# Kernel optimization log

Measured on AMD Instinct MI355X. Metric: run time of the kernel, lower is better.

The kernel has to match this reference:

```python
import jax, jax.numpy as jnp
import numpy as np
import math

DIM = 768
HEADS = 12
HEAD_DIM = DIM // HEADS
LENS_T = 64
LENS_S = 256
NTOK = LENS_T + LENS_S
BATCH = 32
MLP_HIDDEN = 4 * DIM
KEEP_RATIO = 0.7
LENS_KEEP = math.ceil(KEEP_RATIO * LENS_S)  # 180, static
NEG_INF = -1e9  # finite stand-in for masked_fill(-inf); mask is all-False here
LN_EPS = 1e-5


def layer_norm(x, g, b):
    m = jnp.mean(x, axis=-1, keepdims=True)
    v = jnp.var(x, axis=-1, keepdims=True)
    return (x - m) * jax.lax.rsqrt(v + LN_EPS) * g + b


def attention(x_normed, w_qkv, w_proj, b_proj, mask):
    # x_normed: [B,N,C]; torch: qkv Linear (no bias), split heads, softmax(qk*scale), proj
    B, N, C = x_normed.shape
    qkv = (x_normed @ w_qkv.T).reshape(B, N, 3, HEADS, HEAD_DIM)
    qkv = jnp.transpose(qkv, (2, 0, 3, 1, 4))  # [3,B,H,N,Dh]
    q, k, v = qkv[0], qkv[1], qkv[2]
    scores = jnp.einsum('bhqd,bhkd->bhqk', q, k) * (HEAD_DIM ** -0.5)
    scores = jnp.where(mask[:, None, None, :], NEG_INF, scores)
    attn = jax.nn.softmax(scores, axis=-1)  # [B,H,N,N]
    out = jnp.einsum('bhqk,bhkd->bhqd', attn, v)
    out = jnp.transpose(out, (0, 2, 1, 3)).reshape(B, N, C)
    return out @ w_proj.T + b_proj, attn


def mlp(x, w_fc1, b_fc1, w_fc2, b_fc2):
    h = jax.nn.gelu(x @ w_fc1.T + b_fc1, approximate=False)
    return h @ w_fc2.T + b_fc2


def candidate_topk(attn_all, tmpl_mask_f):
    # attn_all: [B,H,N,N]; template->search block, masked mean over template rows,
    # mean over heads, sort descending, split into keep/removed.
    attn_ts = attn_all[:, :, :LENS_T, LENS_T:]  # [B,H,T,S]
    w = tmpl_mask_f[:, None, :, None]  # [B,1,T,1]
    denom = jnp.sum(tmpl_mask_f, axis=1)[:, None, None]  # [B,1,1]
    scores = jnp.sum(attn_ts * w, axis=2) / denom  # [B,H,S] mean over kept template rows
    scores = jnp.mean(scores, axis=1)  # [B,S] mean over heads
    order = jnp.argsort(-scores, axis=1)  # descending
    return order[:, :LENS_KEEP], order[:, LENS_KEEP:]


def gather_tokens(tokens, topk_idx):
    tokens_t = tokens[:, :LENS_T]
    tokens_s = tokens[:, LENS_T:]
    kept = jnp.take_along_axis(tokens_s, topk_idx[:, :, None], axis=1)
    return jnp.concatenate([tokens_t, kept], axis=1)


def setup_inputs() -> dict:
    key = jax.random.key(0)
    ks = jax.random.split(key, 12)
    s = 0.02
    return {
        'x_rgb': jax.random.normal(ks[0], (BATCH, NTOK, DIM), jnp.float32),
        'x_tir': jax.random.normal(ks[1], (BATCH, NTOK, DIM), jnp.float32),
        'global_index_t': jax.random.randint(ks[2], (BATCH, LENS_T), 0, 64).astype(jnp.int64),
        'global_index_s': jax.random.randint(ks[3], (BATCH, LENS_S), 0, 256).astype(jnp.int64),
        'mask': jnp.zeros((BATCH, NTOK), dtype=bool),
        'cte_template_mask': jnp.ones((BATCH, LENS_T), dtype=bool),
        'keep_ratio_search': 0,
        'js_loss': jax.random.normal(ks[4], (1,), jnp.float32),
        'g1': jnp.ones((DIM,), jnp.float32),
        'b1': jnp.zeros((DIM,), jnp.float32),
        'w_qkv': jax.random.normal(ks[5], (3 * DIM, DIM), jnp.float32) * s,
        'w_proj': jax.random.normal(ks[6], (DIM, DIM), jnp.float32) * s,
        'b_proj': jnp.zeros((DIM,), jnp.float32),
        'g2': jnp.ones((DIM,), jnp.float32),
        'b2': jnp.zeros((DIM,), jnp.float32),
        'w_fc1': jax.random.normal(ks[7], (MLP_HIDDEN, DIM), jnp.float32) * s,
        'b_fc1': jnp.zeros((MLP_HIDDEN,), jnp.float32),
        'w_fc2': jax.random.normal(ks[8], (DIM, MLP_HIDDEN), jnp.float32) * s,
        'b_fc2': jnp.zeros((DIM,), jnp.float32),
    }


def reference(x_rgb, x_tir, global_index_t, global_index_s, mask, cte_template_mask,
              keep_ratio_search, js_loss, g1, b1, w_qkv, w_proj, b_proj, g2, b2,
              w_fc1, b_fc1, w_fc2, b_fc2):
    # dual-stream shared-weight attention
    rgb_attn_out, corrmap_rgb = attention(layer_norm(x_rgb, g1, b1), w_qkv, w_proj, b_proj, mask)
    tir_attn_out, corrmap_tir = attention(layer_norm(x_tir, g1, b1), w_qkv, w_proj, b_proj, mask)
    x_rgb = x_rgb + rgb_attn_out  # drop_path = Identity
    x_tir = x_tir + tir_attn_out

    # candidate elimination: both streams use the SAME fused attention map,
    # so the topk is identical for rgb and tir (torch calls it twice, same result)
    attn_all = corrmap_rgb + corrmap_tir
    tmpl_mask_f = cte_template_mask.astype(attn_all.dtype)
    topk_idx, non_topk_idx = candidate_topk(attn_all, tmpl_mask_f)
    x_rgb = gather_tokens(x_rgb, topk_idx)
    x_tir = gather_tokens(x_tir, topk_idx)
    global_index_s_new = jnp.take_along_axis(global_index_s, topk_idx, axis=1)
    removed_index_s = jnp.take_along_axis(global_index_s, non_topk_idx, axis=1)

    x_rgb = x_rgb + mlp(layer_norm(x_rgb, g2, b2), w_fc1, b_fc1, w_fc2, b_fc2)
    x_tir = x_tir + mlp(layer_norm(x_tir, g2, b2), w_fc1, b_fc1, w_fc2, b_fc2)
    return (x_rgb, x_tir, global_index_t, global_index_s_new, removed_index_s,
            corrmap_rgb, corrmap_tir, js_loss)
```

## Files before the change

kernel.cpp:

```cpp
#include <hip/hip_runtime.h>

typedef long long LL;
typedef unsigned short ushort_t;
typedef __attribute__((ext_vector_type(8))) short bfrag;
typedef __attribute__((ext_vector_type(8))) _Float16 hfrag;
typedef __attribute__((ext_vector_type(4))) float facc;
typedef __attribute__((ext_vector_type(4))) unsigned short us4;

constexpr int CDIM  = 768;
constexpr int HEADS = 12;
constexpr int LT    = 64;
constexpr int NTOK  = 320;
constexpr int BATCH = 32;
constexpr int LKEEP = 180;
constexpr int LREM  = 76;
constexpr int NK    = 244;

constexpr LL O_XRGB = 0;
constexpr LL O_XTIR = 5996544;
constexpr LL O_GIT  = 11993088;
constexpr LL O_GSN  = 11995136;
constexpr LL O_REM  = 12000896;
constexpr LL O_CR   = 12003328;
constexpr LL O_CT   = 51324928;
constexpr LL O_JS   = 90646528;

constexpr LL W_X1   = 0;
constexpr LL W_X1G  = 15728640;
constexpr LL W_SC   = 27721728;
constexpr LL W_ORD  = 27738112;
constexpr LL W_XN   = 27746304;
constexpr LL W_QKV  = 35610624;
constexpr LL W_ATT  = 59596800;

constexpr LL SZH = 7864320;

__device__ inline ushort_t cvt_bf16(float f) {
    union { float f; unsigned u; } x; x.f = f;
    unsigned u = x.u + 0x7fffu + ((x.u >> 16) & 1u);
    return (ushort_t)(u >> 16);
}
union h16u { _Float16 h; ushort_t u; };

#define GLL(gp, lp) __builtin_amdgcn_global_load_lds( \
    (const __attribute__((address_space(1))) unsigned int*)(gp), \
    (__attribute__((address_space(3))) unsigned int*)(lp), 16, 0, 0)

template<bool B16OUT>
__global__ __launch_bounds__(256)
void ln_kernel(const float* __restrict__ x, const float* __restrict__ g,
               const float* __restrict__ bta, void* __restrict__ y)
{
    LL row = blockIdx.x;
    const float* xr = x + row * 768;
    int t = threadIdx.x;
    float v0 = xr[t], v1 = xr[t + 256], v2 = xr[t + 512];
    __shared__ float red[256];
    red[t] = v0 + v1 + v2;
    __syncthreads();
    for (int s = 128; s; s >>= 1) { if (t < s) red[t] += red[t + s]; __syncthreads(); }
    float mean = red[0] / 768.0f;
    __syncthreads();
    float d0 = v0 - mean, d1 = v1 - mean, d2 = v2 - mean;
    red[t] = d0 * d0 + d1 * d1 + d2 * d2;
    __syncthreads();
    for (int s = 128; s; s >>= 1) { if (t < s) red[t] += red[t + s]; __syncthreads(); }
    float var = red[0] / 768.0f;
    float rs = 1.0f / sqrtf(var + 1e-5f);
    float o0 = d0 * rs * g[t]       + bta[t];
    float o1 = d1 * rs * g[t + 256] + bta[t + 256];
    float o2 = d2 * rs * g[t + 512] + bta[t + 512];
    if (B16OUT) {
        ushort_t* yr = (ushort_t*)y + row * 768;
        yr[t] = cvt_bf16(o0); yr[t + 256] = cvt_bf16(o1); yr[t + 512] = cvt_bf16(o2);
    } else {
        float* yr = (float*)y + row * 768;
        yr[t] = o0; yr[t + 256] = o1; yr[t + 512] = o2;
    }
}

__global__ __launch_bounds__(256)
void ln_gather(const float* __restrict__ X1, const int* __restrict__ srcmap,
               const float* __restrict__ g, const float* __restrict__ bta,
               ushort_t* __restrict__ y)
{
    int row = blockIdx.x;
    const float* xr = X1 + (LL)srcmap[row] * 768;
    int t = threadIdx.x;
    float v0 = xr[t], v1 = xr[t + 256], v2 = xr[t + 512];
    __shared__ float red[256];
    red[t] = v0 + v1 + v2;
    __syncthreads();
    for (int s = 128; s; s >>= 1) { if (t < s) red[t] += red[t + s]; __syncthreads(); }
    float mean = red[0] / 768.0f;
    __syncthreads();
    float d0 = v0 - mean, d1 = v1 - mean, d2 = v2 - mean;
    red[t] = d0 * d0 + d1 * d1 + d2 * d2;
    __syncthreads();
    for (int s = 128; s; s >>= 1) { if (t < s) red[t] += red[t + s]; __syncthreads(); }
    float var = red[0] / 768.0f;
    float rs = 1.0f / sqrtf(var + 1e-5f);
    ushort_t* yr = y + (LL)row * 768;
    yr[t]       = cvt_bf16(d0 * rs * g[t]       + bta[t]);
    yr[t + 256] = cvt_bf16(d1 * rs * g[t + 256] + bta[t + 256]);
    yr[t + 512] = cvt_bf16(d2 * rs * g[t + 512] + bta[t + 512]);
}

__global__ __launch_bounds__(256)
void ln_f16x2(const float* __restrict__ x, const float* __restrict__ g,
              const float* __restrict__ bta,
              ushort_t* __restrict__ yh, ushort_t* __restrict__ yl)
{
    LL row = blockIdx.x;
    const float* xr = x + row * 768;
    int t = threadIdx.x;
    float v0 = xr[t], v1 = xr[t + 256], v2 = xr[t + 512];
    __shared__ float red[256];
    red[t] = v0 + v1 + v2;
    __syncthreads();
    for (int s = 128; s; s >>= 1) { if (t < s) red[t] += red[t + s]; __syncthreads(); }
    float mean = red[0] / 768.0f;
    __syncthreads();
    float d0 = v0 - mean, d1 = v1 - mean, d2 = v2 - mean;
    red[t] = d0 * d0 + d1 * d1 + d2 * d2;
    __syncthreads();
    for (int s = 128; s; s >>= 1) { if (t < s) red[t] += red[t + s]; __syncthreads(); }
    float var = red[0] / 768.0f;
    float rs = 1.0f / sqrtf(var + 1e-5f);
    #pragma unroll
    for (int c = 0; c < 3; ++c) {
        float d = (c == 0 ? d0 : c == 1 ? d1 : d2);
        int idx = t + c * 256;
        float o = d * rs * g[idx] + bta[idx];
        h16u hi, lo;
        hi.h = (_Float16)o;
        lo.h = (_Float16)(o - (float)hi.h);
        yh[row * 768 + idx] = hi.u;
        yl[row * 768 + idx] = lo.u;
    }
}

__global__ __launch_bounds__(256)
void cvt_f16x2(const float* __restrict__ in, ushort_t* __restrict__ oh,
               ushort_t* __restrict__ ol, int n)
{
    int i = (blockIdx.x * 256 + threadIdx.x) * 4;
    if (i >= n) return;
    float4 v = *(const float4*)(in + i);
    us4 h, l;
    #pragma unroll
    for (int j = 0; j < 4; ++j) {
        float f = (j == 0 ? v.x : j == 1 ? v.y : j == 2 ? v.z : v.w);
        h16u hh, ll;
        hh.h = (_Float16)f;
        ll.h = (_Float16)(f - (float)hh.h);
        h[j] = hh.u; l[j] = ll.u;
    }
    *(us4*)(oh + i) = h;
    *(us4*)(ol + i) = l;
}

__global__ __launch_bounds__(256)
void gemm_qkv(const ushort_t* __restrict__ Ah, const ushort_t* __restrict__ Al,
              const ushort_t* __restrict__ Bh, const ushort_t* __restrict__ Bl,
              ushort_t* __restrict__ Q1, ushort_t* __restrict__ Q2,
              ushort_t* __restrict__ K1, ushort_t* __restrict__ K2,
              ushort_t* __restrict__ Vt)
{
    __shared__ ushort_t Ahs[8192], Als[8192], Bhs[8192], Bls[8192];
    const int t = threadIdx.x;
    const int wave = t >> 6, lane = t & 63;
    const int wr = wave >> 1, wc = wave & 1;
    const int lr = lane & 15, lh = lane >> 4;
    const LL bm = (LL)blockIdx.y * 128, bn = (LL)blockIdx.x * 128;
    const bool vt = (blockIdx.x >= 12);

    facc acc[4][4];
    #pragma unroll
    for (int i = 0; i < 4; ++i)
        #pragma unroll
        for (int j = 0; j < 4; ++j) acc[i][j] = (facc)(0.0f);

    const LL soff = (bm + wave * 16 + (lane >> 2)) * (LL)768 + (lane & 3) * 8;
    const LL boff = (bn + wave * 16 + (lane >> 2)) * (LL)768 + (lane & 3) * 8;
    const LL a64 = (LL)64 * 768;

    GLL(Ah + soff,       &Ahs[wave * 512]);
    GLL(Ah + soff + a64, &Ahs[2048 + wave * 512]);
    GLL(Bh + boff,       &Bhs[wave * 512]);
    GLL(Bh + boff + a64, &Bhs[2048 + wave * 512]);
    if (!vt) {
        GLL(Al + soff,       &Als[wave * 512]);
        GLL(Al + soff + a64, &Als[2048 + wave * 512]);
        GLL(Bl + boff,       &Bls[wave * 512]);
        GLL(Bl + boff + a64, &Bls[2048 + wave * 512]);
    }
    __syncthreads();

    int cur = 0;
    for (int k0 = 0; k0 < 768; k0 += 32) {
        int nb = (cur ^ 1) * 4096;
        if (k0 + 32 < 768) {
            GLL(Ah + soff + k0 + 32,       &Ahs[nb + wave * 512]);
            GLL(Ah + soff + k0 + 32 + a64, &Ahs[nb + 2048 + wave * 512]);
            GLL(Bh + boff + k0 + 32,       &Bhs[nb + wave * 512]);
            GLL(Bh + boff + k0 + 32 + a64, &Bhs[nb + 2048 + wave * 512]);
            if (!vt) {
                GLL(Al + soff + k0 + 32,       &Als[nb + wave * 512]);
                GLL(Al + soff + k0 + 32 + a64, &Als[nb + 2048 + wave * 512]);
                GLL(Bl + boff + k0 + 32,       &Bls[nb + wave * 512]);
                GLL(Bl + boff + k0 + 32 + a64, &Bls[nb + 2048 + wave * 512]);
            }
        }
        int cb = cur * 4096;
        hfrag ah[4], bh[4];
        #pragma unroll
        for (int mi = 0; mi < 4; ++mi)
            ah[mi] = *(const hfrag*)&Ahs[cb + (wr * 64 + mi * 16 + lr) * 32 + lh * 8];
        #pragma unroll
        for (int ni = 0; ni < 4; ++ni)
            bh[ni] = *(const hfrag*)&Bhs[cb + (wc * 64 + ni * 16 + lr) * 32 + lh * 8];
        if (!vt) {
            hfrag al[4], bl[4];
            #pragma unroll
            for (int mi = 0; mi < 4; ++mi)
                al[mi] = *(const hfrag*)&Als[cb + (wr * 64 + mi * 16 + lr) * 32 + lh * 8];
            #pragma unroll
            for (int ni = 0; ni < 4; ++ni)
                bl[ni] = *(const hfrag*)&Bls[cb + (wc * 64 + ni * 16 + lr) * 32 + lh * 8];
            #pragma unroll
            for (int mi = 0; mi < 4; ++mi)
                #pragma unroll
                for (int ni = 0; ni < 4; ++ni) {
                    acc[mi][ni] = __builtin_amdgcn_mfma_f32_16x16x32_f16(al[mi], bh[ni], acc[mi][ni], 0, 0, 0);
                    acc[mi][ni] = __builtin_amdgcn_mfma_f32_16x16x32_f16(ah[mi], bl[ni], acc[mi][ni], 0, 0, 0);
                    acc[mi][ni] = __builtin_amdgcn_mfma_f32_16x16x32_f16(ah[mi], bh[ni], acc[mi][ni], 0, 0, 0);
                }
        } else {
            #pragma unroll
            for (int mi = 0; mi < 4; ++mi)
                #pragma unroll
                for (int ni = 0; ni < 4; ++ni)
                    acc[mi][ni] = __builtin_amdgcn_mfma_f32_16x16x32_f16(ah[mi], bh[ni], acc[mi][ni], 0, 0, 0);
        }
        __syncthreads();
        cur ^= 1;
    }

    #pragma unroll
    for (int mi = 0; mi < 4; ++mi)
        #pragma unroll
        for (int ni = 0; ni < 4; ++ni)
            #pragma unroll
            for (int j = 0; j < 4; ++j) {
                int r = (int)bm + wr * 64 + mi * 16 + lh * 4 + j;
                int c = (int)bn + wc * 64 + ni * 16 + lr;
                int b = r / 320, tt = r - b * 320;
                int s = c / 768, rem = c - s * 768;
                int h = rem >> 6, d = rem & 63;
                LL hb = (LL)(b * 12 + h) * 20480;
                float v = acc[mi][ni][j];
                if (s == 2) {
                    Vt[hb + d * 320 + tt] = cvt_bf16(v);
                } else {
                    h16u a1, a2;
                    a1.h = (_Float16)v;
                    a2.h = (_Float16)(v - (float)a1.h);
                    LL idx = hb + (LL)tt * 64 + d;
                    if (s == 0) { Q1[idx] = a1.u; Q2[idx] = a2.u; }
                    else        { K1[idx] = a1.u; K2[idx] = a2.u; }
                }
            }
}

__global__ __launch_bounds__(256, 2)
void fused_attn(const ushort_t* __restrict__ Qh, const ushort_t* __restrict__ Qm,
                const ushort_t* __restrict__ Kh, const ushort_t* __restrict__ Km,
                const ushort_t* __restrict__ Vt,
                float* __restrict__ corr, ushort_t* __restrict__ attb,
                double* __restrict__ part, int mod)
{
    __shared__ __align__(128) unsigned char lds[81920];
    constexpr int PS = 40960;

    const int t = threadIdx.x;
    const int wave = t >> 6, lane = t & 63;
    const int lr = lane & 15, lh = lane >> 4;
    const int id  = blockIdx.x;
    const int xcd = id & 7;
    const int rem = id >> 3;
    const int grp = rem / 5;
    const int r0i = rem - grp * 5;
    const int bh  = grp * 8 + xcd;
    const int b = bh / 12, h = bh - b * 12;
    const int r0 = r0i * 64;
    const LL kvbase = (LL)bh * 20480;

    const LL qoff = kvbase + (LL)(r0 + wave * 16 + lr) * 64 + lh * 8;
    hfrag qh0 = *(const hfrag*)(Qh + qoff), qh1 = *(const hfrag*)(Qh + qoff + 32);
    hfrag qm0 = *(const hfrag*)(Qm + qoff), qm1 = *(const hfrag*)(Qm + qoff + 32);

    facc sacc[20];
    #pragma unroll
    for (int ct = 0; ct < 20; ++ct) sacc[ct] = (facc)(0.0f);

    #pragma unroll
    for (int ha = 0; ha < 5; ++ha) {
        if (ha) __syncthreads();
        #pragma unroll
        for (int i = 0; i < 4; ++i) {
            int id2 = wave * 4 + i;
            int s = id2 >> 3, c = id2 & 7;
            int local = c * 1024 + lane * 16;
            int row = local >> 7;
            int sb = local ^ ((row & 7) << 4);
            LL src = kvbase + (LL)ha * 4096 + (sb >> 1);
            const ushort_t* kp = (s == 0) ? Kh : Km;
            GLL(kp + src, &lds[s * 8192 + c * 1024]);
        }
        __syncthreads();

        #pragma unroll
        for (int ctl = 0; ctl < 4; ++ctl) {
            int tokl = ctl * 16 + lr;
            int x = (tokl & 7) << 4;
            const unsigned char* kb = lds + tokl * 128;
            int o0 = (lh * 16) ^ x;
            int o1 = (64 + lh * 16) ^ x;
            hfrag kh0 = *(const hfrag*)(kb + o0);
            hfrag kh1 = *(const hfrag*)(kb + o1);
            hfrag km0 = *(const hfrag*)(kb + 8192 + o0);
            hfrag km1 = *(const hfrag*)(kb + 8192 + o1);
            facc a = sacc[ha * 4 + ctl];
            a = __builtin_amdgcn_mfma_f32_16x16x32_f16(qm0, kh0, a, 0, 0, 0);
            a = __builtin_amdgcn_mfma_f32_16x16x32_f16(qh0, km0, a, 0, 0, 0);
            a = __builtin_amdgcn_mfma_f32_16x16x32_f16(qh0, kh0, a, 0, 0, 0);
            a = __builtin_amdgcn_mfma_f32_16x16x32_f16(qm1, kh1, a, 0, 0, 0);
            a = __builtin_amdgcn_mfma_f32_16x16x32_f16(qh1, km1, a, 0, 0, 0);
            a = __builtin_amdgcn_mfma_f32_16x16x32_f16(qh1, kh1, a, 0, 0, 0);
            sacc[ha * 4 + ctl] = a;
        }
    }

    __syncthreads();

    #pragma unroll
    for (int i = 0; i < 10; ++i) {
        int chunk = wave * 10 + i;
        int gs = chunk * 1024 + lane * 16;
        int d = gs / 640;
        int w = gs - d * 640;
        int sb = d * 640 + (w ^ ((d & 7) << 4));
        GLL(Vt + kvbase + (sb >> 1), &lds[chunk * 1024]);
    }

    float rs4[4];
    #pragma unroll
    for (int j = 0; j < 4; ++j) {
        float m = sacc[0][j];
        #pragma unroll
        for (int ct = 1; ct < 20; ++ct) m = fmaxf(m, sacc[ct][j]);
        #pragma unroll
        for (int o = 1; o < 16; o <<= 1) m = fmaxf(m, __shfl_xor(m, o, 64));
        m *= 0.125f;
        float s = 0.0f;
        #pragma unroll
        for (int ct = 0; ct < 20; ++ct) {
            float e = expf(sacc[ct][j] * 0.125f - m);
            sacc[ct][j] = e;
            s += e;
        }
        #pragma unroll
        for (int o = 1; o < 16; o <<= 1) s += __shfl_xor(s, o, 64);
        float rs = 1.0f / s;
        rs4[j] = rs;

        int prow = wave * 16 + lh * 4 + j;
        int xr = (prow & 7) << 4;
        #pragma unroll
        for (int ct = 0; ct < 20; ++ct) {
            int pcol = ct * 16 + lr;
            *(ushort_t*)(lds + PS + prow * 640 + ((pcol * 2) ^ xr)) =
                cvt_bf16(sacc[ct][j] * rs);
        }
    }

    __syncthreads();

    facc oacc[4];
    #pragma unroll
    for (int dt = 0; dt < 4; ++dt) oacc[dt] = (facc)(0.0f);
    int prow2 = wave * 16 + lr;
    int xp = (prow2 & 7) << 4;
    #pragma unroll
    for (int k0 = 0; k0 < 10; ++k0) {
        bfrag pa = *(const bfrag*)(lds + PS + prow2 * 640 + ((k0 * 64 + lh * 16) ^ xp));
        #pragma unroll
        for (int dt = 0; dt < 4; ++dt) {
            int dcol = dt * 16 + lr;
            bfrag vb = *(const bfrag*)(lds + dcol * 640 + ((k0 * 64 + lh * 16) ^ ((dcol & 7) << 4)));
            oacc[dt] = __builtin_amdgcn_mfma_f32_16x16x32_bf16(pa, vb, oacc[dt], 0, 0, 0);
        }
    }
    #pragma unroll
    for (int dt = 0; dt < 4; ++dt)
        #pragma unroll
        for (int j = 0; j < 4; ++j) {
            int grow = r0 + wave * 16 + lh * 4 + j;
            int gcol = h * 64 + dt * 16 + lr;
            attb[(LL)(b * 320 + grow) * 768 + gcol] = cvt_bf16(oacc[dt][j]);
        }

    __syncthreads();

    #pragma unroll
    for (int ct = 0; ct < 20; ++ct) {
        int pcol = ct * 16 + lr;
        #pragma unroll
        for (int j = 0; j < 4; ++j) {
            int prow = wave * 16 + lh * 4 + j;
            *(float*)(lds + (prow * 320 + pcol) * 4) = sacc[ct][j] * rs4[j];
        }
    }
    __syncthreads();

    float* crow = corr + (LL)bh * 102400 + (LL)r0 * 320;
    #pragma unroll
    for (int i = 0; i < 20; ++i) {
        int idx = i * 256 + t;
        int row = idx / 80, c4 = idx - row * 80;
        float4 v = *(const float4*)(lds + (row * 320 + c4 * 4) * 4);
        *(float4*)(crow + row * 320 + c4 * 4) = v;
    }

    if (r0i == 0) {
        double s64 = 0.0;
        for (int r = 0; r < 64; ++r)
            s64 += (double)*(const float*)(lds + (r * 320 + 64 + t) * 4);
        part[((LL)mod * 384 + bh) * 256 + t] = s64;
    }
}

template<int EPI>
__global__ __launch_bounds__(256)
void gemm_mfma(const ushort_t* __restrict__ A, const ushort_t* __restrict__ B,
               void* __restrict__ Cv, const float* __restrict__ bias,
               const float* __restrict__ res, const int* __restrict__ rmap,
               int K, int lda, int ldb, int ldc, int ldres)
{
    __shared__ ushort_t As[8192];
    __shared__ ushort_t Bs[8192];
    const int t = threadIdx.x;
    const int wave = t >> 6, lane = t & 63;
    const int wr = wave >> 1, wc = wave & 1;
    const LL bm = (LL)blockIdx.y * 128, bn = (LL)blockIdx.x * 128;

    facc acc[4][4];
    #pragma unroll
    for (int i = 0; i < 4; ++i)
        #pragma unroll
        for (int j = 0; j < 4; ++j) acc[i][j] = (facc)(0.0f);

    const int lr = lane & 15, lh = lane >> 4;
    const ushort_t* gA = A + (bm + wave * 16 + (lane >> 2)) * lda + (lane & 3) * 8;
    const ushort_t* gB = B + (bn + wave * 16 + (lane >> 2)) * ldb + (lane & 3) * 8;
    const LL a64 = (LL)64 * lda, b64 = (LL)64 * ldb;

    GLL(gA,        &As[wave * 512]);
    GLL(gA + a64,  &As[2048 + wave * 512]);
    GLL(gB,        &Bs[wave * 512]);
    GLL(gB + b64,  &Bs[2048 + wave * 512]);
    __syncthreads();

    int cur = 0;
    for (int k0 = 0; k0 < K; k0 += 32) {
        int nb = (cur ^ 1) * 4096;
        if (k0 + 32 < K) {
            GLL(gA + k0 + 32,        &As[nb + wave * 512]);
            GLL(gA + k0 + 32 + a64,  &As[nb + 2048 + wave * 512]);
            GLL(gB + k0 + 32,        &Bs[nb + wave * 512]);
            GLL(gB + k0 + 32 + b64,  &Bs[nb + 2048 + wave * 512]);
        }
        int cb = cur * 4096;
        bfrag a[4], b[4];
        #pragma unroll
        for (int m = 0; m < 4; ++m)
            a[m] = *(const bfrag*)&As[cb + (wr * 64 + m * 16 + lr) * 32 + lh * 8];
        #pragma unroll
        for (int n = 0; n < 4; ++n)
            b[n] = *(const bfrag*)&Bs[cb + (wc * 64 + n * 16 + lr) * 32 + lh * 8];
        #pragma unroll
        for (int m = 0; m < 4; ++m)
            #pragma unroll
            for (int n = 0; n < 4; ++n)
                acc[m][n] = __builtin_amdgcn_mfma_f32_16x16x32_bf16(a[m], b[n], acc[m][n], 0, 0, 0);
        __syncthreads();
        cur ^= 1;
    }

    #pragma unroll
    for (int m = 0; m < 4; ++m) {
        #pragma unroll
        for (int n = 0; n < 4; ++n) {
            #pragma unroll
            for (int j = 0; j < 4; ++j) {
                LL r = bm + wr * 64 + m * 16 + lh * 4 + j;
                LL c = bn + wc * 64 + n * 16 + lr;
                float v = acc[m][n][j] + bias[c];
                if (EPI == 1) {
                    v = 0.5f * v * (erff(v * 0.70710678118654752f) + 1.0f);
                    ((ushort_t*)Cv)[r * ldc + c] = cvt_bf16(v);
                } else {
                    LL rr = rmap ? (LL)rmap[r] : r;
                    v += res[rr * ldres + c];
                    ((float*)Cv)[r * ldc + c] = v;
                }
            }
        }
    }
}

__global__ __launch_bounds__(256)
void f32_to_bf16(const float* __restrict__ in, ushort_t* __restrict__ out, int n)
{
    int i = (blockIdx.x * 256 + threadIdx.x) * 4;
    if (i >= n) return;
    float4 v = *(const float4*)(in + i);
    us4 o;
    o[0] = cvt_bf16(v.x); o[1] = cvt_bf16(v.y);
    o[2] = cvt_bf16(v.z); o[3] = cvt_bf16(v.w);
    *(us4*)(out + i) = o;
}

__global__ __launch_bounds__(256)
void score_combine(const double* __restrict__ part, double* __restrict__ scores)
{
    int b = blockIdx.x, j = threadIdx.x;
    double acc = 0.0;
    for (int h = 0; h < 12; ++h) {
        LL i0 = ((LL)(b * 12 + h)) * 256 + j;
        acc += (part[i0] + part[98304 + i0]) / 64.0;
    }
    scores[b * 256 + j] = acc / 12.0;
}

__global__ __launch_bounds__(256)
void rank_kernel(const double* __restrict__ scores, const int* __restrict__ gis,
                 int* __restrict__ ord, float* __restrict__ onew, float* __restrict__ orem)
{
    int b = blockIdx.x, j = threadIdx.x;
    __shared__ double s[256];
    s[j] = scores[b * 256 + j];
    __syncthreads();
    double sj = s[j];
    int r = 0;
    for (int i = 0; i < 256; ++i) {
        double si = s[i];
        r += (si > sj) || (si == sj && i < j);
    }
    ord[b * 256 + r] = j;
    float gv = (float)gis[b * 256 + j];
    if (r < LKEEP) onew[b * LKEEP + r] = gv;
    else           orem[b * LREM + (r - LKEEP)] = gv;
}

__global__ __launch_bounds__(256)
void build_srcmap(const int* __restrict__ ord, int* __restrict__ srcmap)
{
    int r = blockIdx.x * 256 + threadIdx.x;
    if (r >= 2 * BATCH * NK) return;
    int m = r / (BATCH * NK);
    int rem = r - m * (BATCH * NK);
    int b = rem / NK;
    int rr = rem - b * NK;
    int src = (rr < LT) ? rr : (LT + ord[b * 256 + (rr - LT)]);
    srcmap[r] = m * (BATCH * NTOK) + b * NTOK + src;
}

__global__ void copy_misc(const int* __restrict__ git, const float* __restrict__ js,
                          float* __restrict__ out)
{
    int i = blockIdx.x * 256 + threadIdx.x;
    if (i < 2048)      out[O_GIT + i] = (float)git[i];
    else if (i == 2048) out[O_JS] = js[0];
}

extern "C" void kernel_launch(void* const* d_in, const int* in_sizes, int n_in,
                              void* d_out, int out_size, void* d_ws, size_t ws_size,
                              hipStream_t stream)
{
    const float* xin_m[2] = { (const float*)d_in[0], (const float*)d_in[1] };
    const int*   git    = (const int*)d_in[2];
    const int*   gis    = (const int*)d_in[3];
    const float* js     = (const float*)d_in[7];
    const float* g1     = (const float*)d_in[8];
    const float* b1     = (const float*)d_in[9];
    const float* w_qkv  = (const float*)d_in[10];
    const float* w_proj = (const float*)d_in[11];
    const float* b_proj = (const float*)d_in[12];
    const float* g2     = (const float*)d_in[13];
    const float* b2     = (const float*)d_in[14];
    const float* w_fc1  = (const float*)d_in[15];
    const float* b_fc1  = (const float*)d_in[16];
    const float* w_fc2  = (const float*)d_in[17];
    const float* b_fc2  = (const float*)d_in[18];

    float* out = (float*)d_out;
    float* ws  = (float*)d_ws;

    double* sc  = (double*)(ws + W_SC);
    int*    ord = (int*)(ws + W_ORD);

    ushort_t* Xh  = (ushort_t*)(ws + W_XN);
    ushort_t* Xl  = Xh + SZH;
    ushort_t* ATTb = (ushort_t*)(ws + W_XN);
    ushort_t* QK  = (ushort_t*)(ws + W_QKV);
    ushort_t* Qh2 = QK,           *Qm2 = QK + SZH;
    ushort_t* Kh2 = QK + 2 * SZH, *Km2 = QK + 3 * SZH;
    ushort_t* Wh  = (ushort_t*)(ws + W_ATT);
    ushort_t* Wl  = Wh + 1769472;
    ushort_t* Vt  = (ushort_t*)(ws + W_ATT + 2000000);
    double*   part = (double*)(ws + W_ATT + 6000000);
    int*      srcmap = (int*)(ws + W_ATT + 6000000 + 393216);
    ushort_t* WPROJb = (ushort_t*)(ws + W_X1G);
    ushort_t* WFC1b  = (ushort_t*)(ws + W_ATT);
    ushort_t* WFC2b  = (ushort_t*)(ws + W_ATT + 1179648);
    ushort_t* XN2b   = (ushort_t*)(ws + W_XN);
    ushort_t* H1b    = (ushort_t*)(ws + W_QKV);

    f32_to_bf16<<<dim3(576), dim3(256), 0, stream>>>(w_proj, WPROJb, 589824);
    cvt_f16x2<<<dim3(1728), dim3(256), 0, stream>>>(w_qkv, Wh, Wl, 1769472);

    for (int m = 0; m < 2; ++m) {
        const float* xin = xin_m[m];
        float* corr = out + (m ? O_CT : O_CR);
        float* X1m  = ws + W_X1 + (LL)m * BATCH * NTOK * CDIM;

        ln_f16x2<<<dim3(BATCH * NTOK), dim3(256), 0, stream>>>(xin, g1, b1, Xh, Xl);

        gemm_qkv<<<dim3(18, 80), dim3(256), 0, stream>>>(
            Xh, Xl, Wh, Wl, Qh2, Qm2, Kh2, Km2, Vt);

        fused_attn<<<dim3(1920), dim3(256), 0, stream>>>(
            Qh2, Qm2, Kh2, Km2, Vt, corr, ATTb, part, m);

        gemm_mfma<2><<<dim3(6, 80), dim3(256), 0, stream>>>(
            ATTb, WPROJb, X1m, b_proj, xin, nullptr, 768, 768, 768, 768, 768);
    }

    score_combine<<<dim3(BATCH), dim3(256), 0, stream>>>(part, sc);
    rank_kernel<<<dim3(BATCH), dim3(256), 0, stream>>>(sc, gis, ord,
                                                       out + O_GSN, out + O_REM);
    build_srcmap<<<dim3(61), dim3(256), 0, stream>>>(ord, srcmap);
    copy_misc<<<dim3(9), dim3(256), 0, stream>>>(git, js, out);

    f32_to_bf16<<<dim3(2304), dim3(256), 0, stream>>>(w_fc1, WFC1b, 2359296);
    f32_to_bf16<<<dim3(2304), dim3(256), 0, stream>>>(w_fc2, WFC2b, 2359296);

    ln_gather<<<dim3(2 * BATCH * NK), dim3(256), 0, stream>>>(
        ws + W_X1, srcmap, g2, b2, XN2b);

    gemm_mfma<1><<<dim3(24, 122), dim3(256), 0, stream>>>(
        XN2b, WFC1b, H1b, b_fc1, nullptr, nullptr, 768, 768, 768, 3072, 0);

    gemm_mfma<2><<<dim3(6, 122), dim3(256), 0, stream>>>(
        H1b, WFC2b, out + O_XRGB, b_fc2, ws + W_X1, srcmap, 3072, 3072, 3072, 768, 768);
}
```

Measured before the change: 957.7 us.

## Defer projection GEMM until after token ranking; use 32x32 MFMA tiles

The attention output projection now runs after the top-k ranking, only on the 244 kept tokens per batch, using a row map that gathers attention rows and residual inputs. This drops the projection work for eliminated tokens and lets the second LayerNorm read compacted rows directly. The GEMM switches from 16x16x32 to 32x32x16 bf16 MFMA with a different LDS layout. The score, rank, srcmap and misc-copy kernels are merged into one launch. Both attention outputs now need separate buffers, and the workspace is reused differently (Xh now lives in the X1 region).

```diff
diff --git a/kernel.cpp b/kernel.cpp
--- a/kernel.cpp
+++ b/kernel.cpp
@@ -5,6 +5,7 @@
 typedef __attribute__((ext_vector_type(8))) short bfrag;
 typedef __attribute__((ext_vector_type(8))) _Float16 hfrag;
 typedef __attribute__((ext_vector_type(4))) float facc;
+typedef __attribute__((ext_vector_type(16))) float facc16;
 typedef __attribute__((ext_vector_type(4))) unsigned short us4;
 
 constexpr int CDIM  = 768;
@@ -77,33 +78,6 @@
         float* yr = (float*)y + row * 768;
         yr[t] = o0; yr[t + 256] = o1; yr[t + 512] = o2;
     }
-}
-
-__global__ __launch_bounds__(256)
-void ln_gather(const float* __restrict__ X1, const int* __restrict__ srcmap,
-               const float* __restrict__ g, const float* __restrict__ bta,
-               ushort_t* __restrict__ y)
-{
-    int row = blockIdx.x;
-    const float* xr = X1 + (LL)srcmap[row] * 768;
-    int t = threadIdx.x;
-    float v0 = xr[t], v1 = xr[t + 256], v2 = xr[t + 512];
-    __shared__ float red[256];
-    red[t] = v0 + v1 + v2;
-    __syncthreads();
-    for (int s = 128; s; s >>= 1) { if (t < s) red[t] += red[t + s]; __syncthreads(); }
-    float mean = red[0] / 768.0f;
-    __syncthreads();
-    float d0 = v0 - mean, d1 = v1 - mean, d2 = v2 - mean;
-    red[t] = d0 * d0 + d1 * d1 + d2 * d2;
-    __syncthreads();
-    for (int s = 128; s; s >>= 1) { if (t < s) red[t] += red[t + s]; __syncthreads(); }
-    float var = red[0] / 768.0f;
-    float rs = 1.0f / sqrtf(var + 1e-5f);
-    ushort_t* yr = y + (LL)row * 768;
-    yr[t]       = cvt_bf16(d0 * rs * g[t]       + bta[t]);
-    yr[t + 256] = cvt_bf16(d1 * rs * g[t + 256] + bta[t + 256]);
-    yr[t + 512] = cvt_bf16(d2 * rs * g[t + 512] + bta[t + 512]);
 }
 
 __global__ __launch_bounds__(256)
@@ -443,75 +417,83 @@
 
 template<int EPI>
 __global__ __launch_bounds__(256)
-void gemm_mfma(const ushort_t* __restrict__ A, const ushort_t* __restrict__ B,
-               void* __restrict__ Cv, const float* __restrict__ bias,
-               const float* __restrict__ res, const int* __restrict__ rmap,
-               int K, int lda, int ldb, int ldc, int ldres)
+void gemm_mfma32(const ushort_t* __restrict__ A, const ushort_t* __restrict__ B,
+                 void* __restrict__ Cv, const float* __restrict__ bias,
+                 const float* __restrict__ res, const int* __restrict__ amap,
+                 int K, int lda, int ldb, int ldc, int ldres)
 {
     __shared__ ushort_t As[8192];
     __shared__ ushort_t Bs[8192];
     const int t = threadIdx.x;
     const int wave = t >> 6, lane = t & 63;
     const int wr = wave >> 1, wc = wave & 1;
+    const int l31 = lane & 31, lg = lane >> 5;
     const LL bm = (LL)blockIdx.y * 128, bn = (LL)blockIdx.x * 128;
 
-    facc acc[4][4];
-    #pragma unroll
-    for (int i = 0; i < 4; ++i)
-        #pragma unroll
-        for (int j = 0; j < 4; ++j) acc[i][j] = (facc)(0.0f);
-
-    const int lr = lane & 15, lh = lane >> 4;
-    const ushort_t* gA = A + (bm + wave * 16 + (lane >> 2)) * lda + (lane & 3) * 8;
-    const ushort_t* gB = B + (bn + wave * 16 + (lane >> 2)) * ldb + (lane & 3) * 8;
-    const LL a64 = (LL)64 * lda, b64 = (LL)64 * ldb;
-
-    GLL(gA,        &As[wave * 512]);
-    GLL(gA + a64,  &As[2048 + wave * 512]);
-    GLL(gB,        &Bs[wave * 512]);
-    GLL(gB + b64,  &Bs[2048 + wave * 512]);
+    facc16 acc[2][2];
+    #pragma unroll
+    for (int i = 0; i < 2; ++i)
+        #pragma unroll
+        for (int j = 0; j < 2; ++j) acc[i][j] = (facc16)(0.0f);
+
+    const int strow = wave * 32 + (lane >> 1);
+    int garow = (int)bm + strow;
+    if (amap) garow = amap[garow];
+    const LL abase = (LL)garow * lda + (lane & 1) * 8;
+    const LL bbase = (bn + strow) * (LL)ldb + (lane & 1) * 8;
+
+    GLL(A + abase,      &As[wave * 512]);
+    GLL(A + abase + 16, &As[2048 + wave * 512]);
+    GLL(B + bbase,      &Bs[wave * 512]);
+    GLL(B + bbase + 16, &Bs[2048 + wave * 512]);
     __syncthreads();
 
     int cur = 0;
     for (int k0 = 0; k0 < K; k0 += 32) {
         int nb = (cur ^ 1) * 4096;
         if (k0 + 32 < K) {
-            GLL(gA + k0 + 32,        &As[nb + wave * 512]);
-            GLL(gA + k0 + 32 + a64,  &As[nb + 2048 + wave * 512]);
-            GLL(gB + k0 + 32,        &Bs[nb + wave * 512]);
-            GLL(gB + k0 + 32 + b64,  &Bs[nb + 2048 + wave * 512]);
+            GLL(A + abase + k0 + 32,      &As[nb + wave * 512]);
+            GLL(A + abase + k0 + 48,      &As[nb + 2048 + wave * 512]);
+            GLL(B + bbase + k0 + 32,      &Bs[nb + wave * 512]);
+            GLL(B + bbase + k0 + 48,      &Bs[nb + 2048 + wave * 512]);
         }
         int cb = cur * 4096;
-        bfrag a[4], b[4];
-        #pragma unroll
-        for (int m = 0; m < 4; ++m)
-            a[m] = *(const bfrag*)&As[cb + (wr * 64 + m * 16 + lr) * 32 + lh * 8];
-        #pragma unroll
-        for (int n = 0; n < 4; ++n)
-            b[n] = *(const bfrag*)&Bs[cb + (wc * 64 + n * 16 + lr) * 32 + lh * 8];
-        #pragma unroll
-        for (int m = 0; m < 4; ++m)
-            #pragma unroll
-            for (int n = 0; n < 4; ++n)
-                acc[m][n] = __builtin_amdgcn_mfma_f32_16x16x32_bf16(a[m], b[n], acc[m][n], 0, 0, 0);
+        bfrag a[2][2], b[2][2];
+        #pragma unroll
+        for (int mt = 0; mt < 2; ++mt)
+            #pragma unroll
+            for (int kh = 0; kh < 2; ++kh)
+                a[mt][kh] = *(const bfrag*)&As[cb + kh * 2048 + (wr * 64 + mt * 32 + l31) * 16 + lg * 8];
+        #pragma unroll
+        for (int nt = 0; nt < 2; ++nt)
+            #pragma unroll
+            for (int kh = 0; kh < 2; ++kh)
+                b[nt][kh] = *(const bfrag*)&Bs[cb + kh * 2048 + (wc * 64 + nt * 32 + l31) * 16 + lg * 8];
+        #pragma unroll
+        for (int kh = 0; kh < 2; ++kh)
+            #pragma unroll
+            for (int mt = 0; mt < 2; ++mt)
+                #pragma unroll
+                for (int nt = 0; nt < 2; ++nt)
+                    acc[mt][nt] = __builtin_amdgcn_mfma_f32_32x32x16_bf16(a[mt][kh], b[nt][kh], acc[mt][nt], 0, 0, 0);
         __syncthreads();
         cur ^= 1;
     }
 
     #pragma unroll
-    for (int m = 0; m < 4; ++m) {
-        #pragma unroll
-        for (int n = 0; n < 4; ++n) {
-            #pragma unroll
-            for (int j = 0; j < 4; ++j) {
-                LL r = bm + wr * 64 + m * 16 + lh * 4 + j;
-                LL c = bn + wc * 64 + n * 16 + lr;
-                float v = acc[m][n][j] + bias[c];
+    for (int mt = 0; mt < 2; ++mt) {
+        #pragma unroll
+        for (int nt = 0; nt < 2; ++nt) {
+            #pragma unroll
+            for (int rg = 0; rg < 16; ++rg) {
+                LL r = bm + wr * 64 + mt * 32 + (rg & 3) + 8 * (rg >> 2) + 4 * lg;
+                LL c = bn + wc * 64 + nt * 32 + l31;
+                float v = acc[mt][nt][rg] + bias[c];
                 if (EPI == 1) {
                     v = 0.5f * v * (erff(v * 0.70710678118654752f) + 1.0f);
                     ((ushort_t*)Cv)[r * ldc + c] = cvt_bf16(v);
                 } else {
-                    LL rr = rmap ? (LL)rmap[r] : r;
+                    LL rr = amap ? (LL)amap[r] : r;
                     v += res[rr * ldres + c];
                     ((float*)Cv)[r * ldc + c] = v;
                 }
@@ -533,7 +515,9 @@
 }
 
 __global__ __launch_bounds__(256)
-void score_combine(const double* __restrict__ part, double* __restrict__ scores)
+void rank_all(const double* __restrict__ part, const int* __restrict__ gis,
+              const int* __restrict__ git, const float* __restrict__ js,
+              int* __restrict__ srcmap, float* __restrict__ out)
 {
     int b = blockIdx.x, j = threadIdx.x;
     double acc = 0.0;
@@ -541,48 +525,27 @@
         LL i0 = ((LL)(b * 12 + h)) * 256 + j;
         acc += (part[i0] + part[98304 + i0]) / 64.0;
     }
-    scores[b * 256 + j] = acc / 12.0;
-}
-
-__global__ __launch_bounds__(256)
-void rank_kernel(const double* __restrict__ scores, const int* __restrict__ gis,
-                 int* __restrict__ ord, float* __restrict__ onew, float* __restrict__ orem)
-{
-    int b = blockIdx.x, j = threadIdx.x;
+    double sj = acc / 12.0;
     __shared__ double s[256];
-    s[j] = scores[b * 256 + j];
-    __syncthreads();
-    double sj = s[j];
+    __shared__ int sord[256];
+    s[j] = sj;
+    __syncthreads();
     int r = 0;
     for (int i = 0; i < 256; ++i) {
         double si = s[i];
         r += (si > sj) || (si == sj && i < j);
     }
-    ord[b * 256 + r] = j;
+    sord[r] = j;
     float gv = (float)gis[b * 256 + j];
-    if (r < LKEEP) onew[b * LKEEP + r] = gv;
-    else           orem[b * LREM + (r - LKEEP)] = gv;
-}
-
-__global__ __launch_bounds__(256)
-void build_srcmap(const int* __restrict__ ord, int* __restrict__ srcmap)
-{
-    int r = blockIdx.x * 256 + threadIdx.x;
-    if (r >= 2 * BATCH * NK) return;
-    int m = r / (BATCH * NK);
-    int rem = r - m * (BATCH * NK);
-    int b = rem / NK;
-    int rr = rem - b * NK;
-    int src = (rr < LT) ? rr : (LT + ord[b * 256 + (rr - LT)]);
-    srcmap[r] = m * (BATCH * NTOK) + b * NTOK + src;
-}
-
-__global__ void copy_misc(const int* __restrict__ git, const float* __restrict__ js,
-                          float* __restrict__ out)
-{
-    int i = blockIdx.x * 256 + threadIdx.x;
-    if (i < 2048)      out[O_GIT + i] = (float)git[i];
-    else if (i == 2048) out[O_JS] = js[0];
+    if (r < LKEEP) out[O_GSN + b * LKEEP + r] = gv;
+    else           out[O_REM + b * LREM + (r - LKEEP)] = gv;
+    __syncthreads();
+    if (j < NK) {
+        int src = (j < LT) ? j : (LT + sord[j - LT]);
+        srcmap[b * NK + j] = b * NTOK + src;
+    }
+    if (j < 64) out[O_GIT + b * 64 + j] = (float)git[b * 64 + j];
+    if (b == 0 && j == 0) out[O_JS] = js[0];
 }
 
 extern "C" void kernel_launch(void* const* d_in, const int* in_sizes, int n_in,
@@ -608,12 +571,11 @@
     float* out = (float*)d_out;
     float* ws  = (float*)d_ws;
 
-    double* sc  = (double*)(ws + W_SC);
-    int*    ord = (int*)(ws + W_ORD);
-
-    ushort_t* Xh  = (ushort_t*)(ws + W_XN);
-    ushort_t* Xl  = Xh + SZH;
-    ushort_t* ATTb = (ushort_t*)(ws + W_XN);
+    ushort_t* Xh   = (ushort_t*)(ws + W_X1);
+    ushort_t* Xl   = Xh + SZH;
+    float*    X1c  = ws + W_X1;
+    ushort_t* ATTb0 = (ushort_t*)(ws + W_XN);
+    ushort_t* ATTb1 = ATTb0 + SZH;
     ushort_t* QK  = (ushort_t*)(ws + W_QKV);
     ushort_t* Qh2 = QK,           *Qm2 = QK + SZH;
     ushort_t* Kh2 = QK + 2 * SZH, *Km2 = QK + 3 * SZH;
@@ -621,7 +583,7 @@
     ushort_t* Wl  = Wh + 1769472;
     ushort_t* Vt  = (ushort_t*)(ws + W_ATT + 2000000);
     double*   part = (double*)(ws + W_ATT + 6000000);
-    int*      srcmap = (int*)(ws + W_ATT + 6000000 + 393216);
+    int*      srcmap = (int*)(ws + W_ATT + 6400000);
     ushort_t* WPROJb = (ushort_t*)(ws + W_X1G);
     ushort_t* WFC1b  = (ushort_t*)(ws + W_ATT);
     ushort_t* WFC2b  = (ushort_t*)(ws + W_ATT + 1179648);
@@ -634,7 +596,7 @@
     for (int m = 0; m < 2; ++m) {
         const float* xin = xin_m[m];
         float* corr = out + (m ? O_CT : O_CR);
-        float* X1m  = ws + W_X1 + (LL)m * BATCH * NTOK * CDIM;
+        ushort_t* ATTbm = m ? ATTb1 : ATTb0;
 
         ln_f16x2<<<dim3(BATCH * NTOK), dim3(256), 0, stream>>>(xin, g1, b1, Xh, Xl);
 
@@ -642,27 +604,26 @@
             Xh, Xl, Wh, Wl, Qh2, Qm2, Kh2, Km2, Vt);
 
         fused_attn<<<dim3(1920), dim3(256), 0, stream>>>(
-            Qh2, Qm2, Kh2, Km2, Vt, corr, ATTb, part, m);
-
-        gemm_mfma<2><<<dim3(6, 80), dim3(256), 0, stream>>>(
-            ATTb, WPROJb, X1m, b_proj, xin, nullptr, 768, 768, 768, 768, 768);
-    }
-
-    score_combine<<<dim3(BATCH), dim3(256), 0, stream>>>(part, sc);
-    rank_kernel<<<dim3(BATCH), dim3(256), 0, stream>>>(sc, gis, ord,
-                                                       out + O_GSN, out + O_REM);
-    build_srcmap<<<dim3(61), dim3(256), 0, stream>>>(ord, srcmap);
-    copy_misc<<<dim3(9), dim3(256), 0, stream>>>(git, js, out);
+            Qh2, Qm2, Kh2, Km2, Vt, corr, ATTbm, part, m);
+    }
 
     f32_to_bf16<<<dim3(2304), dim3(256), 0, stream>>>(w_fc1, WFC1b, 2359296);
     f32_to_bf16<<<dim3(2304), dim3(256), 0, stream>>>(w_fc2, WFC2b, 2359296);
 
-    ln_gather<<<dim3(2 * BATCH * NK), dim3(256), 0, stream>>>(
-        ws + W_X1, srcmap, g2, b2, XN2b);
-
-    gemm_mfma<1><<<dim3(24, 122), dim3(256), 0, stream>>>(
+    rank_all<<<dim3(BATCH), dim3(256), 0, stream>>>(part, gis, git, js, srcmap, out);
+
+    for (int m = 0; m < 2; ++m) {
+        gemm_mfma32<2><<<dim3(6, 61), dim3(256), 0, stream>>>(
+            m ? ATTb1 : ATTb0, WPROJb, X1c + (LL)m * 5996544, b_proj,
+            xin_m[m], srcmap, 768, 768, 768, 768, 768);
+    }
+
+    ln_kernel<true><<<dim3(2 * BATCH * NK), dim3(256), 0, stream>>>(
+        X1c, g2, b2, XN2b);
+
+    gemm_mfma32<1><<<dim3(24, 122), dim3(256), 0, stream>>>(
         XN2b, WFC1b, H1b, b_fc1, nullptr, nullptr, 768, 768, 768, 3072, 0);
 
-    gemm_mfma<2><<<dim3(6, 122), dim3(256), 0, stream>>>(
-        H1b, WFC2b, out + O_XRGB, b_fc2, ws + W_X1, srcmap, 3072, 3072, 3072, 768, 768);
-}
+    gemm_mfma32<2><<<dim3(6, 122), dim3(256), 0, stream>>>(
+        H1b, WFC2b, out + O_XRGB, b_fc2, X1c, nullptr, 3072, 3072, 3072, 768, 768);
+}
```

Measured after the change: 1.014 ms. +5.8%, slower.
